# Kernel tuning notes

Hardware: AMD Instinct MI355X
Metric: run time of the kernel (lower is better)

Reference implementation:

```python
import jax, jax.numpy as jnp
import numpy as np

BINS = 10


def setup_inputs() -> dict:
    key = jax.random.key(0)
    k1, k2 = jax.random.split(key)
    pred = jax.random.normal(k1, (16384, 4096), dtype=jnp.float32)
    target = jax.random.randint(k2, (16384, 4096), 0, 2).astype(jnp.float32)
    return {"pred": pred, "target": target}


def reference(pred, target):
    bins = BINS
    # edges = [0, 0.1, ..., 1.0], last edge bumped by 1e-6 (as in torch module)
    edges = jnp.arange(bins + 1, dtype=jnp.float32) / bins
    edges = edges.at[-1].add(1e-6)

    # gradient magnitude g = |pred.detach() - target|
    g = jnp.abs(jax.lax.stop_gradient(pred) - target)

    # label_weight is forced to all-ones in the original forward -> all valid
    tot = jnp.float32(g.size)

    # histogram binning: element e belongs to bin i iff edges[i] <= g < edges[i+1]
    gf = g.ravel()
    idx = jnp.searchsorted(edges, gf, side="right") - 1  # in [-1, bins]
    in_range = (idx >= 0) & (idx < bins)                  # g >= 1+1e-6 falls outside
    idxc = jnp.clip(idx, 0, bins - 1)
    counts = jnp.zeros(bins, jnp.float32).at[idxc].add(in_range.astype(jnp.float32))

    n = jnp.sum(counts > 0).astype(jnp.float32)  # number of non-empty bins
    cnt_e = counts[idxc]                          # per-element bin count
    per = jnp.where(in_range & (cnt_e > 0), tot / jnp.maximum(cnt_e, 1.0), 0.0)
    weights = (per / jnp.maximum(n, 1.0)).reshape(pred.shape)

    # weighted BCE with logits, reduction='sum', normalized by tot
    log_p = jax.nn.log_sigmoid(pred)
    log_np = jax.nn.log_sigmoid(-pred)
    loss = -jnp.sum(weights * (target * log_p + (1.0 - target) * log_np)) / tot
    return loss
```

## Files before the change

kernel.cpp:

```cpp
#include <hip/hip_runtime.h>


#define THREADS 256
#define LSTRIDE 11
#define NB 10

__device__ __forceinline__ float bce(float x, float t) {
    return fmaxf(x, 0.0f) - x * t + __logf(1.0f + __expf(-fabsf(x)));
}

__global__ __launch_bounds__(THREADS) void ghmc_partial(
    const float4* __restrict__ p4, const float4* __restrict__ t4, int n4,
    const float* __restrict__ p1, const float* __restrict__ t1, long long ntot,
    double* __restrict__ g_sum, unsigned int* __restrict__ g_cnt) {

    __shared__ float lds[THREADS * LSTRIDE];
    const int tid = threadIdx.x;
    float* slots = &lds[tid * LSTRIDE];
#pragma unroll
    for (int b = 0; b < LSTRIDE; ++b) slots[b] = 0.0f;

    const float EDGE10 = 1.0f + 1e-6f;
    unsigned long long ca = 0ull, cb = 0ull;
    unsigned cnt[NB];
#pragma unroll
    for (int b = 0; b < NB; ++b) cnt[b] = 0u;

    auto put = [&](float x, float t, unsigned long long& c) {
        const float g = fabsf(x - t);
        const float l = bce(x, t);
        int idx = (int)(g * 10.0f);
        idx = idx > 9 ? 9 : idx;
        idx = (g < EDGE10) ? idx : 10;
        c += 1ull << (6 * idx);
        slots[idx] += l;
    };
    auto flushc = [&](unsigned long long& c) {
#pragma unroll
        for (int b = 0; b < NB; ++b) cnt[b] += (unsigned)((c >> (6 * b)) & 63ull);
        c = 0ull;
    };

    const int stride = gridDim.x * blockDim.x;
    int i = blockIdx.x * blockDim.x + tid;
    const int iters = n4 / stride;

    float4 p, t;
    if (iters > 0) { p = p4[i]; t = t4[i]; }
    for (int it = 0; it < iters; ++it) {
        const int inext = i + stride;
        float4 pn, tn;
        if (it + 1 < iters) { pn = p4[inext]; tn = t4[inext]; }
        put(p.x, t.x, ca); put(p.y, t.y, cb);
        put(p.z, t.z, ca); put(p.w, t.w, cb);
        p = pn; t = tn; i = inext;
    }
    flushc(ca); flushc(cb);

    for (; i < n4; i += stride) {
        const float4 pp = p4[i], tt = t4[i];
        put(pp.x, tt.x, ca); put(pp.y, tt.y, cb);
        put(pp.z, tt.z, ca); put(pp.w, tt.w, cb);
        flushc(ca); flushc(cb);
    }
    if (blockIdx.x == 0 && tid == 0) {
        for (long long j = (long long)n4 * 4; j < ntot; ++j) {
            const float x = p1[j], tt = t1[j];
            const float g = fabsf(x - tt);
            if (g < EDGE10) {
                int idx = (int)(g * 10.0f);
                idx = idx > 9 ? 9 : idx;
                atomicAdd(&g_sum[idx], (double)bce(x, tt));
                atomicAdd(&g_cnt[idx], 1u);
            }
        }
    }

    float s[NB];
#pragma unroll
    for (int b = 0; b < NB; ++b) s[b] = slots[b];

#pragma unroll
    for (int off = 32; off > 0; off >>= 1) {
#pragma unroll
        for (int b = 0; b < NB; ++b) {
            s[b] += __shfl_down(s[b], off, 64);
            cnt[b] += __shfl_down(cnt[b], off, 64);
        }
    }

    __shared__ float w_sum[4][NB];
    __shared__ unsigned w_cnt[4][NB];
    const int wave = tid >> 6;
    const int lane = tid & 63;
    if (lane == 0) {
#pragma unroll
        for (int b = 0; b < NB; ++b) { w_sum[wave][b] = s[b]; w_cnt[wave][b] = cnt[b]; }
    }
    __syncthreads();
    if (tid < NB) {
        const float fs = w_sum[0][tid] + w_sum[1][tid] + w_sum[2][tid] + w_sum[3][tid];
        const unsigned fc = w_cnt[0][tid] + w_cnt[1][tid] + w_cnt[2][tid] + w_cnt[3][tid];
        atomicAdd(&g_sum[tid], (double)fs);
        atomicAdd(&g_cnt[tid], fc);
    }
}

__global__ void ghmc_final(const double* __restrict__ g_sum,
                           const unsigned int* __restrict__ g_cnt,
                           float* __restrict__ out) {
    if (blockIdx.x == 0 && threadIdx.x == 0) {
        double loss = 0.0;
        int n = 0;
#pragma unroll
        for (int b = 0; b < NB; ++b) {
            const unsigned c = g_cnt[b];
            if (c > 0u) {
                n += 1;
                loss += g_sum[b] / (double)c;
            }
        }
        loss /= (n > 0) ? (double)n : 1.0;
        out[0] = (float)loss;
    }
}

extern "C" void kernel_launch(void* const* d_in, const int* in_sizes, int n_in,
                              void* d_out, int out_size, void* d_ws, size_t ws_size,
                              hipStream_t stream) {
    const float* pred = (const float*)d_in[0];
    const float* tgt  = (const float*)d_in[1];
    long long ntot = (long long)in_sizes[0];
    int n4 = (int)(ntot / 4);

    double* g_sum = (double*)d_ws;
    unsigned int* g_cnt = (unsigned int*)((char*)d_ws + NB * sizeof(double));

    hipMemsetAsync(d_ws, 0, NB * sizeof(double) + NB * sizeof(unsigned int),
                   stream);

    const int threads = THREADS;
    const int blocks = 4096;
    hipLaunchKernelGGL(ghmc_partial, dim3(blocks), dim3(threads), 0, stream,
                       (const float4*)pred, (const float4*)tgt, n4,
                       pred, tgt, ntot, g_sum, g_cnt);
    hipLaunchKernelGGL(ghmc_final, dim3(1), dim3(64), 0, stream,
                       g_sum, g_cnt, (float*)d_out);
}
```

Baseline: 545.1 us.

## Use contiguous per-block chunks with deeper multi-float4 prefetch and fewer blocks

Each block now processes one contiguous chunk instead of a grid-stride loop, and prefetches four float4 pairs per thread per iteration into registers. Bin counts go to four packed 64-bit counters that are flushed every 15 groups to avoid 6-bit field overflow. The grid is halved to 2048 blocks. The aim is more memory-level parallelism and fewer per-block reduction atomics, at the cost of higher register pressure and possible occupancy loss.

```diff
diff --git a/kernel.cpp b/kernel.cpp
--- a/kernel.cpp
+++ b/kernel.cpp
@@ -4,6 +4,7 @@
 #define THREADS 256
 #define LSTRIDE 11
 #define NB 10
+#define PF 4
 
 __device__ __forceinline__ float bce(float x, float t) {
     return fmaxf(x, 0.0f) - x * t + __logf(1.0f + __expf(-fabsf(x)));
@@ -21,7 +22,7 @@
     for (int b = 0; b < LSTRIDE; ++b) slots[b] = 0.0f;
 
     const float EDGE10 = 1.0f + 1e-6f;
-    unsigned long long ca = 0ull, cb = 0ull;
+    unsigned long long cc[4] = {0ull, 0ull, 0ull, 0ull};
     unsigned cnt[NB];
 #pragma unroll
     for (int b = 0; b < NB; ++b) cnt[b] = 0u;
@@ -35,34 +36,67 @@
         c += 1ull << (6 * idx);
         slots[idx] += l;
     };
-    auto flushc = [&](unsigned long long& c) {
+    auto flush_all = [&]() {
 #pragma unroll
-        for (int b = 0; b < NB; ++b) cnt[b] += (unsigned)((c >> (6 * b)) & 63ull);
-        c = 0ull;
+        for (int q = 0; q < 4; ++q) {
+#pragma unroll
+            for (int b = 0; b < NB; ++b)
+                cnt[b] += (unsigned)((cc[q] >> (6 * b)) & 63ull);
+            cc[q] = 0ull;
+        }
     };
 
-    const int stride = gridDim.x * blockDim.x;
-    int i = blockIdx.x * blockDim.x + tid;
-    const int iters = n4 / stride;
+    const int chunk = (n4 + (int)gridDim.x - 1) / (int)gridDim.x;
+    const int start = blockIdx.x * chunk;
+    const int end = min(start + chunk, n4);
+    const int count = max(end - start, 0);
+    const int full = count / THREADS;
+    const int ngrp = full / PF;
 
-    float4 p, t;
-    if (iters > 0) { p = p4[i]; t = t4[i]; }
-    for (int it = 0; it < iters; ++it) {
-        const int inext = i + stride;
-        float4 pn, tn;
-        if (it + 1 < iters) { pn = p4[inext]; tn = t4[inext]; }
-        put(p.x, t.x, ca); put(p.y, t.y, cb);
-        put(p.z, t.z, ca); put(p.w, t.w, cb);
-        p = pn; t = tn; i = inext;
+    float4 P[PF], T[PF], Pn[PF], Tn[PF];
+    if (ngrp > 0) {
+#pragma unroll
+        for (int g = 0; g < PF; ++g) {
+            const int id = start + g * THREADS + tid;
+            P[g] = p4[id]; T[g] = t4[id];
+        }
     }
-    flushc(ca); flushc(cb);
+    for (int g2 = 0; g2 < ngrp; ++g2) {
+        const int nb = start + (g2 + 1) * PF * THREADS + tid;
+        if (g2 + 1 < ngrp) {
+#pragma unroll
+            for (int g = 0; g < PF; ++g) {
+                Pn[g] = p4[nb + g * THREADS];
+                Tn[g] = t4[nb + g * THREADS];
+            }
+        }
+#pragma unroll
+        for (int g = 0; g < PF; ++g) {
+            put(P[g].x, T[g].x, cc[0]);
+            put(P[g].y, T[g].y, cc[1]);
+            put(P[g].z, T[g].z, cc[2]);
+            put(P[g].w, T[g].w, cc[3]);
+        }
+        if ((g2 % 15) == 14) flush_all();
+#pragma unroll
+        for (int g = 0; g < PF; ++g) { P[g] = Pn[g]; T[g] = Tn[g]; }
+    }
+    for (int k = ngrp * PF; k < full; ++k) {
+        const int id = start + k * THREADS + tid;
+        const float4 pp = p4[id], tt = t4[id];
+        put(pp.x, tt.x, cc[0]); put(pp.y, tt.y, cc[1]);
+        put(pp.z, tt.z, cc[2]); put(pp.w, tt.w, cc[3]);
+    }
+    {
+        const int id = start + full * THREADS + tid;
+        if (id < end) {
+            const float4 pp = p4[id], tt = t4[id];
+            put(pp.x, tt.x, cc[0]); put(pp.y, tt.y, cc[1]);
+            put(pp.z, tt.z, cc[2]); put(pp.w, tt.w, cc[3]);
+        }
+    }
+    flush_all();
 
-    for (; i < n4; i += stride) {
-        const float4 pp = p4[i], tt = t4[i];
-        put(pp.x, tt.x, ca); put(pp.y, tt.y, cb);
-        put(pp.z, tt.z, ca); put(pp.w, tt.w, cb);
-        flushc(ca); flushc(cb);
-    }
     if (blockIdx.x == 0 && tid == 0) {
         for (long long j = (long long)n4 * 4; j < ntot; ++j) {
             const float x = p1[j], tt = t1[j];
@@ -79,7 +113,6 @@
     float s[NB];
 #pragma unroll
     for (int b = 0; b < NB; ++b) s[b] = slots[b];
-
 #pragma unroll
     for (int off = 32; off > 0; off >>= 1) {
 #pragma unroll
@@ -140,7 +173,7 @@
                    stream);
 
     const int threads = THREADS;
-    const int blocks = 4096;
+    const int blocks = 2048;
     hipLaunchKernelGGL(ghmc_partial, dim3(blocks), dim3(threads), 0, stream,
                        (const float4*)pred, (const float4*)tgt, n4,
                        pred, tgt, ntot, g_sum, g_cnt);
```

After: 519.9 us. 1.05x faster.
